# Optimization experiments

Measured on AMD Instinct MI355X. Metric: run time of the kernel, lower is better.

## Reference

```python
import jax, jax.numpy as jnp
import numpy as np

B, S, D = 1, 2048, 2048
H, HD = 32, 64  # num_heads, head_dim = hidden_size // num_heads


def setup_inputs() -> dict:
    key = jax.random.key(0)
    ks = jax.random.split(key, 7)
    sc = 0.02
    return {
        "hidden_states": jax.random.normal(ks[0], (B, S, D), dtype=jnp.float32),
        "Wq": jax.random.normal(ks[1], (D, D), dtype=jnp.float32) * sc,
        "Wk": jax.random.normal(ks[2], (D, D), dtype=jnp.float32) * sc,
        "Wv": jax.random.normal(ks[3], (D, D), dtype=jnp.float32) * sc,
        "Wf": jax.random.normal(ks[4], (H, D), dtype=jnp.float32) * sc,
        "bf": jax.random.normal(ks[5], (H,), dtype=jnp.float32),
        "Wo": jax.random.normal(ks[6], (D, D), dtype=jnp.float32) * sc,
    }


def reference(hidden_states, Wq, Wk, Wv, Wf, bf, Wo):
    x = hidden_states
    b, s, _ = x.shape
    # projections (nn.Linear: x @ W^T)
    q = (x @ Wq.T).reshape(b, s, H, HD)
    k = (x @ Wk.T).reshape(b, s, H, HD)
    v = (x @ Wv.T).reshape(b, s, H, HD)
    # per-head log forget gates, computed in float32 as in the torch module
    f = jax.nn.log_sigmoid((x @ Wf.T + bf).astype(jnp.float32))  # [b, s, H]
    # cumulative log decay; FoX bias D_ij = F_i - F_j (sum of log gates over (j, i])
    Fcum = jnp.cumsum(f, axis=1)               # [b, s, H]
    Fh = jnp.transpose(Fcum, (0, 2, 1))        # [b, H, s]
    scale = HD ** -0.5
    scores = jnp.einsum('bqhd,bkhd->bhqk', q, k).astype(jnp.float32) * scale
    scores = scores + Fh[:, :, :, None] - Fh[:, :, None, :]
    causal = jnp.tril(jnp.ones((s, s), dtype=bool))
    scores = jnp.where(causal[None, None], scores, -jnp.inf)
    p = jax.nn.softmax(scores, axis=-1).astype(q.dtype)  # [b, H, q, k]
    o = jnp.einsum('bhqk,bkhd->bqhd', p, v).reshape(b, s, D)
    return o @ Wo.T
```

## Files before the change

### kernel.cpp

```cpp
#include <hip/hip_runtime.h>
#include <stdint.h>

#define SEQ 2048
#define DM  2048
#define NH  32
#define HDIM 64

typedef unsigned short u16;
typedef short bf16x8 __attribute__((ext_vector_type(8)));
typedef float f32x4 __attribute__((ext_vector_type(4)));

__device__ __forceinline__ u16 f2bf(float f) {
    union { float f; uint32_t u; } v; v.f = f;
    uint32_t u = v.u;
    uint32_t r = (u + 0x7fffu + ((u >> 16) & 1u)) >> 16;
    return (u16)r;
}

#define GLOAD_LDS16(g, l) __builtin_amdgcn_global_load_lds( \
    (const __attribute__((address_space(1))) uint32_t*)(g), \
    (__attribute__((address_space(3))) uint32_t*)(l), 16, 0, 0)

__global__ __launch_bounds__(256) void cvt_bf16(
    const float* __restrict__ X, const float* __restrict__ Wq,
    const float* __restrict__ Wk, const float* __restrict__ Wv,
    const float* __restrict__ Wo,
    u16* __restrict__ Xb, u16* __restrict__ Wqb, u16* __restrict__ Wkb,
    u16* __restrict__ Wvb, u16* __restrict__ Wob)
{
    const int NV = (DM * SEQ) / 4;
    int idx = blockIdx.x * blockDim.x + threadIdx.x;
    int total = NV * 5;
    for (; idx < total; idx += gridDim.x * blockDim.x) {
        int arr = idx / NV, i = idx - arr * NV;
        const float4* s; u16* d;
        switch (arr) {
            case 0:  s = (const float4*)X;  d = Xb;  break;
            case 1:  s = (const float4*)Wq; d = Wqb; break;
            case 2:  s = (const float4*)Wk; d = Wkb; break;
            case 3:  s = (const float4*)Wv; d = Wvb; break;
            default: s = (const float4*)Wo; d = Wob; break;
        }
        float4 v = s[i];
        ushort4 o;
        o.x = f2bf(v.x); o.y = f2bf(v.y); o.z = f2bf(v.z); o.w = f2bf(v.w);
        *(ushort4*)(d + i * 4) = o;
    }
}

__global__ __launch_bounds__(256) void gates_gemm(
    const float* __restrict__ X, const float* __restrict__ Wf,
    float* __restrict__ Fpart)
{
    __shared__ float lX[64 * 68];
    __shared__ float lW[32 * 68];
    int s0 = blockIdx.x * 64;
    int kp = blockIdx.y;
    int tid = threadIdx.x;
    int h = tid & 31, sg = tid >> 5;
    float acc[8] = {0.f,0.f,0.f,0.f,0.f,0.f,0.f,0.f};
    for (int k0 = kp * 128; k0 < kp * 128 + 128; k0 += 64) {
        __syncthreads();
        {
            int r = tid >> 2, seg = tid & 3;
            const float4* src = (const float4*)(X + (size_t)(s0 + r) * DM + k0);
            float4* dst = (float4*)(&lX[r * 68]);
#pragma unroll
            for (int i = 0; i < 4; i++) dst[seg + 4 * i] = src[seg + 4 * i];
#pragma unroll
            for (int j = 0; j < 2; j++) {
                int ii = tid + j * 256;
                int wr_ = ii >> 4, wc_ = ii & 15;
                ((float4*)(&lW[wr_ * 68]))[wc_] =
                    ((const float4*)(Wf + (size_t)wr_ * DM + k0))[wc_];
            }
        }
        __syncthreads();
#pragma unroll
        for (int k4 = 0; k4 < 16; k4++) {
            float4 w = ((const float4*)(&lW[h * 68]))[k4];
#pragma unroll
            for (int i = 0; i < 8; i++) {
                float4 x = ((const float4*)(&lX[(sg + 8 * i) * 68]))[k4];
                acc[i] += x.x * w.x + x.y * w.y + x.z * w.z + x.w * w.w;
            }
        }
    }
#pragma unroll
    for (int i = 0; i < 8; i++)
        Fpart[(size_t)kp * NH * SEQ + h * SEQ + s0 + sg + 8 * i] = acc[i];
}

__global__ __launch_bounds__(256) void gates_scan(
    const float* __restrict__ Fpart, float* __restrict__ F,
    const float* __restrict__ bfp)
{
    __shared__ float lws[4];
    int h = blockIdx.x;
    int tid = threadIdx.x;
    int lane = tid & 63, wv = tid >> 6;
    float bb = bfp[h];
    float v[8] = {0.f,0.f,0.f,0.f,0.f,0.f,0.f,0.f};
#pragma unroll
    for (int kp = 0; kp < 16; kp++) {
        const float4* src = (const float4*)(Fpart + (size_t)kp * NH * SEQ + (size_t)h * SEQ);
        float4 a = src[tid * 2], b2 = src[tid * 2 + 1];
        v[0] += a.x;  v[1] += a.y;  v[2] += a.z;  v[3] += a.w;
        v[4] += b2.x; v[5] += b2.y; v[6] += b2.z; v[7] += b2.w;
    }
#pragma unroll
    for (int i = 0; i < 8; i++) {
        float g = v[i] + bb;
        v[i] = fminf(g, 0.f) - log1pf(expf(-fabsf(g)));
    }
#pragma unroll
    for (int i = 1; i < 8; i++) v[i] += v[i - 1];
    float tsum = v[7];
    float sc = tsum;
#pragma unroll
    for (int d = 1; d < 64; d <<= 1) {
        float t = __shfl_up(sc, d);
        if (lane >= d) sc += t;
    }
    if (lane == 63) lws[wv] = sc;
    __syncthreads();
    float woff = 0.f;
#pragma unroll
    for (int w2 = 0; w2 < 4; w2++) if (w2 < wv) woff += lws[w2];
    float off = woff + sc - tsum;
#pragma unroll
    for (int i = 0; i < 8; i++) v[i] += off;
    float4 o1 = {v[0], v[1], v[2], v[3]}, o2 = {v[4], v[5], v[6], v[7]};
    ((float4*)(F + (size_t)h * SEQ))[tid * 2] = o1;
    ((float4*)(F + (size_t)h * SEQ))[tid * 2 + 1] = o2;
}

__global__ __launch_bounds__(256, 3) void gemm_qkv(
    const u16* __restrict__ A,
    const u16* __restrict__ B0, const u16* __restrict__ B1, const u16* __restrict__ B2,
    u16* __restrict__ C0, u16* __restrict__ C1, u16* __restrict__ C2)
{
    __shared__ u16 lA[128 * 32];
    __shared__ u16 lB[128 * 32];
    const int K = DM, N = DM;
    int z = blockIdx.z;
    const u16* Bm = (z == 0) ? B0 : ((z == 1) ? B1 : B2);
    u16* Cm = (z == 0) ? C0 : ((z == 1) ? C1 : C2);
    int m0 = blockIdx.y * 128, n0 = blockIdx.x * 128;
    int tid = threadIdx.x;
    int wave = tid >> 6, lane = tid & 63, ln = lane & 15, quad = lane >> 4;
    int wr = (wave >> 1) * 64, wc = (wave & 1) * 64;

    f32x4 acc[4][4];
#pragma unroll
    for (int i = 0; i < 4; i++)
#pragma unroll
        for (int j = 0; j < 4; j++)
#pragma unroll
            for (int r = 0; r < 4; r++) acc[i][j][r] = 0.f;

    int srow = wave * 32 + (lane >> 2);
    int scol = (lane & 3) * 8;
    const u16* gA0 = &A[(size_t)(m0 + srow) * K + scol];
    const u16* gA1 = &A[(size_t)(m0 + srow + 16) * K + scol];
    const u16* gB0 = &Bm[(size_t)(n0 + srow) * K + scol];
    const u16* gB1 = &Bm[(size_t)(n0 + srow + 16) * K + scol];
    u16* dA0 = &lA[(wave * 32) * 32];
    u16* dA1 = &lA[(wave * 32 + 16) * 32];
    u16* dB0 = &lB[(wave * 32) * 32];
    u16* dB1 = &lB[(wave * 32 + 16) * 32];

    for (int kk0 = 0; kk0 < K / 32; kk0++) {
        __syncthreads();
        GLOAD_LDS16(gA0, dA0);
        GLOAD_LDS16(gA1, dA1);
        GLOAD_LDS16(gB0, dB0);
        GLOAD_LDS16(gB1, dB1);
        gA0 += 32; gA1 += 32; gB0 += 32; gB1 += 32;
        __syncthreads();
        bf16x8 af[4], bfr[4];
#pragma unroll
        for (int i = 0; i < 4; i++) af[i]  = *(const bf16x8*)(&lA[(wr + i * 16 + ln) * 32 + quad * 8]);
#pragma unroll
        for (int j = 0; j < 4; j++) bfr[j] = *(const bf16x8*)(&lB[(wc + j * 16 + ln) * 32 + quad * 8]);
#pragma unroll
        for (int i = 0; i < 4; i++)
#pragma unroll
            for (int j = 0; j < 4; j++)
                acc[i][j] = __builtin_amdgcn_mfma_f32_16x16x32_bf16(af[i], bfr[j], acc[i][j], 0, 0, 0);
    }

#pragma unroll
    for (int i = 0; i < 4; i++)
#pragma unroll
        for (int j = 0; j < 4; j++)
#pragma unroll
            for (int r = 0; r < 4; r++) {
                int row = m0 + wr + i * 16 + quad * 4 + r;
                int col = n0 + wc + j * 16 + ln;
                Cm[(size_t)row * N + col] = f2bf(acc[i][j][r]);
            }
}

__global__ __launch_bounds__(256, 3) void gemm_out(
    const u16* __restrict__ A, const u16* __restrict__ B,
    float* __restrict__ C)
{
    __shared__ u16 lA[128 * 32];
    __shared__ u16 lB[128 * 32];
    const int K = DM, N = DM;
    int m0 = blockIdx.y * 128, n0 = blockIdx.x * 128;
    int tid = threadIdx.x;
    int wave = tid >> 6, lane = tid & 63, ln = lane & 15, quad = lane >> 4;
    int wr = (wave >> 1) * 64, wc = (wave & 1) * 64;

    f32x4 acc[4][4];
#pragma unroll
    for (int i = 0; i < 4; i++)
#pragma unroll
        for (int j = 0; j < 4; j++)
#pragma unroll
            for (int r = 0; r < 4; r++) acc[i][j][r] = 0.f;

    int srow = wave * 32 + (lane >> 2);
    int scol = (lane & 3) * 8;
    const u16* gA0 = &A[(size_t)(m0 + srow) * K + scol];
    const u16* gA1 = &A[(size_t)(m0 + srow + 16) * K + scol];
    const u16* gB0 = &B[(size_t)(n0 + srow) * K + scol];
    const u16* gB1 = &B[(size_t)(n0 + srow + 16) * K + scol];
    u16* dA0 = &lA[(wave * 32) * 32];
    u16* dA1 = &lA[(wave * 32 + 16) * 32];
    u16* dB0 = &lB[(wave * 32) * 32];
    u16* dB1 = &lB[(wave * 32 + 16) * 32];

    for (int kk0 = 0; kk0 < K / 32; kk0++) {
        __syncthreads();
        GLOAD_LDS16(gA0, dA0);
        GLOAD_LDS16(gA1, dA1);
        GLOAD_LDS16(gB0, dB0);
        GLOAD_LDS16(gB1, dB1);
        gA0 += 32; gA1 += 32; gB0 += 32; gB1 += 32;
        __syncthreads();
        bf16x8 af[4], bfr[4];
#pragma unroll
        for (int i = 0; i < 4; i++) af[i]  = *(const bf16x8*)(&lA[(wr + i * 16 + ln) * 32 + quad * 8]);
#pragma unroll
        for (int j = 0; j < 4; j++) bfr[j] = *(const bf16x8*)(&lB[(wc + j * 16 + ln) * 32 + quad * 8]);
#pragma unroll
        for (int i = 0; i < 4; i++)
#pragma unroll
            for (int j = 0; j < 4; j++)
                acc[i][j] = __builtin_amdgcn_mfma_f32_16x16x32_bf16(af[i], bfr[j], acc[i][j], 0, 0, 0);
    }

#pragma unroll
    for (int i = 0; i < 4; i++)
#pragma unroll
        for (int j = 0; j < 4; j++)
#pragma unroll
            for (int r = 0; r < 4; r++) {
                int row = m0 + wr + i * 16 + quad * 4 + r;
                int col = n0 + wc + j * 16 + ln;
                C[(size_t)row * N + col] = acc[i][j][r];
            }
}

__global__ __launch_bounds__(256, 2) void attn_fox(
    const u16* __restrict__ Q, const u16* __restrict__ K,
    const u16* __restrict__ V, const float* __restrict__ F,
    u16* __restrict__ O)
{
    __shared__ u16 lK[64 * 72];
    __shared__ u16 lV[64 * 72];
    __shared__ u16 lP[4 * 16 * 72];
    __shared__ float lFq[64];
    __shared__ float lFk[64];

    int h = blockIdx.y;
    int q0 = blockIdx.x * 64;
    int tid = threadIdx.x;
    int wave = tid >> 6, lane = tid & 63, ln = lane & 15, quad = lane >> 4;
    const float scale = 0.125f;

    bf16x8 aq[2];
    int qrow = q0 + wave * 16 + ln;
#pragma unroll
    for (int kk = 0; kk < 2; kk++)
        aq[kk] = *(const bf16x8*)(&Q[(size_t)qrow * DM + h * HDIM + kk * 32 + quad * 8]);

    if (tid < 64) lFq[tid] = F[h * SEQ + q0 + tid];

    float m_run[4], l_run[4];
    f32x4 o_acc[4];
#pragma unroll
    for (int r = 0; r < 4; r++) { m_run[r] = -1e30f; l_run[r] = 0.f; }
#pragma unroll
    for (int jo = 0; jo < 4; jo++)
#pragma unroll
        for (int r = 0; r < 4; r++) o_acc[jo][r] = 0.f;

    float Fq0 = F[h * SEQ + q0];
    int nt = q0 / 64 + 1;
    u16* lPw = &lP[wave * 16 * 72];

    for (int kt = 0; kt < nt; kt++) {
        int kb = kt * 64;
        if (kt < nt - 1) {
            float Fkend = F[h * SEQ + kb + 63];
            if (Fq0 - Fkend < -50.f) continue;
        }
        __syncthreads();
        {
            int row = tid >> 3, seg = tid & 7;
            *(uint4*)(&lK[row * 72 + seg * 8])        = *(const uint4*)(&K[(size_t)(kb + row) * DM + h * HDIM + seg * 8]);
            *(uint4*)(&lK[(row + 32) * 72 + seg * 8]) = *(const uint4*)(&K[(size_t)(kb + row + 32) * DM + h * HDIM + seg * 8]);
        }
#pragma unroll
        for (int half = 0; half < 2; half++) {
            int job = half * 256 + tid;
            int kv = job & 63, hs = job >> 6;
            union { uint4 v; u16 e[8]; } tmp;
            tmp.v = *(const uint4*)(&V[(size_t)(kb + kv) * DM + h * HDIM + hs * 8]);
#pragma unroll
            for (int u = 0; u < 8; u++) lV[(hs * 8 + u) * 72 + kv] = tmp.e[u];
        }
        if (tid < 64) lFk[tid] = F[h * SEQ + kb + tid];
        __syncthreads();

        f32x4 s_acc[4];
#pragma unroll
        for (int j = 0; j < 4; j++)
#pragma unroll
            for (int r = 0; r < 4; r++) s_acc[j][r] = 0.f;
#pragma unroll
        for (int kk = 0; kk < 2; kk++)
#pragma unroll
            for (int j = 0; j < 4; j++) {
                bf16x8 bk = *(const bf16x8*)(&lK[(j * 16 + ln) * 72 + kk * 32 + quad * 8]);
                s_acc[j] = __builtin_amdgcn_mfma_f32_16x16x32_bf16(aq[kk], bk, s_acc[j], 0, 0, 0);
            }

        bool diag = (kt == nt - 1);
        int qbase = q0 + wave * 16 + quad * 4;
        float vv[4][4];
        float m_new[4];
#pragma unroll
        for (int r = 0; r < 4; r++) m_new[r] = -1e30f;
#pragma unroll
        for (int j = 0; j < 4; j++) {
            float fk = lFk[j * 16 + ln];
            int kglob = kb + j * 16 + ln;
#pragma unroll
            for (int r = 0; r < 4; r++) {
                float fq = lFq[wave * 16 + quad * 4 + r];
                float v = s_acc[j][r] * scale + (fq - fk);
                if (diag && kglob > qbase + r) v = -1e30f;
                vv[j][r] = v;
                m_new[r] = fmaxf(m_new[r], v);
            }
        }
#pragma unroll
        for (int r = 0; r < 4; r++) {
#pragma unroll
            for (int m = 1; m < 16; m <<= 1) m_new[r] = fmaxf(m_new[r], __shfl_xor(m_new[r], m));
        }
        float alpha[4];
#pragma unroll
        for (int r = 0; r < 4; r++) {
            float mt = fmaxf(m_run[r], m_new[r]);
            alpha[r] = expf(m_run[r] - mt);
            m_run[r] = mt;
        }
        float lsum[4] = {0.f, 0.f, 0.f, 0.f};
#pragma unroll
        for (int j = 0; j < 4; j++)
#pragma unroll
            for (int r = 0; r < 4; r++) {
                float pv = expf(vv[j][r] - m_run[r]);
                vv[j][r] = pv;
                lsum[r] += pv;
            }
#pragma unroll
        for (int r = 0; r < 4; r++) {
#pragma unroll
            for (int m = 1; m < 16; m <<= 1) lsum[r] += __shfl_xor(lsum[r], m);
            l_run[r] = l_run[r] * alpha[r] + lsum[r];
        }
#pragma unroll
        for (int jo = 0; jo < 4; jo++)
#pragma unroll
            for (int r = 0; r < 4; r++) o_acc[jo][r] *= alpha[r];

#pragma unroll
        for (int j = 0; j < 4; j++)
#pragma unroll
            for (int r = 0; r < 4; r++)
                lPw[(quad * 4 + r) * 72 + j * 16 + ln] = f2bf(vv[j][r]);
        __syncthreads();
        bf16x8 ap[2];
#pragma unroll
        for (int kk = 0; kk < 2; kk++)
            ap[kk] = *(const bf16x8*)(&lPw[ln * 72 + kk * 32 + quad * 8]);
#pragma unroll
        for (int kk = 0; kk < 2; kk++)
#pragma unroll
            for (int jo = 0; jo < 4; jo++) {
                bf16x8 bv = *(const bf16x8*)(&lV[(jo * 16 + ln) * 72 + kk * 32 + quad * 8]);
                o_acc[jo] = __builtin_amdgcn_mfma_f32_16x16x32_bf16(ap[kk], bv, o_acc[jo], 0, 0, 0);
            }
    }

#pragma unroll
    for (int r = 0; r < 4; r++) {
        float inv = 1.f / l_run[r];
        int row = q0 + wave * 16 + quad * 4 + r;
#pragma unroll
        for (int jo = 0; jo < 4; jo++)
            O[(size_t)row * DM + h * HDIM + jo * 16 + ln] = f2bf(o_acc[jo][r] * inv);
    }
}

extern "C" void kernel_launch(void* const* d_in, const int* in_sizes, int n_in,
                              void* d_out, int out_size, void* d_ws, size_t ws_size,
                              hipStream_t stream)
{
    const float* X   = (const float*)d_in[0];
    const float* Wq  = (const float*)d_in[1];
    const float* Wk  = (const float*)d_in[2];
    const float* Wv  = (const float*)d_in[3];
    const float* Wf  = (const float*)d_in[4];
    const float* bfp = (const float*)d_in[5];
    const float* Wo  = (const float*)d_in[6];
    float* out = (float*)d_out;

    char* ws = (char*)d_ws;
    const size_t MB8 = (size_t)DM * SEQ * 2;
    u16* Xb  = (u16*)(ws + 0 * MB8);
    u16* Wqb = (u16*)(ws + 1 * MB8);
    u16* Wkb = (u16*)(ws + 2 * MB8);
    u16* Wvb = (u16*)(ws + 3 * MB8);
    u16* Wob = (u16*)(ws + 4 * MB8);
    u16* Qb  = (u16*)(ws + 5 * MB8);
    u16* Kb  = (u16*)(ws + 6 * MB8);
    u16* Vb  = (u16*)(ws + 7 * MB8);
    u16* Ob  = (u16*)(ws + 8 * MB8);
    float* Fb = (float*)(ws + 9 * MB8);
    float* Fpart = (float*)(ws + 8 * MB8);

    cvt_bf16<<<dim3(4096), dim3(256), 0, stream>>>(X, Wq, Wk, Wv, Wo, Xb, Wqb, Wkb, Wvb, Wob);
    gates_gemm<<<dim3(32, 16), dim3(256), 0, stream>>>(X, Wf, Fpart);
    gates_scan<<<dim3(NH), dim3(256), 0, stream>>>(Fpart, Fb, bfp);
    gemm_qkv<<<dim3(16, 16, 3), dim3(256), 0, stream>>>(Xb, Wqb, Wkb, Wvb, Qb, Kb, Vb);
    attn_fox<<<dim3(SEQ / 64, NH), dim3(256), 0, stream>>>(Qb, Kb, Vb, Fb, Ob);
    gemm_out<<<dim3(16, 16), dim3(256), 0, stream>>>(Ob, Wob, out);
}
```

Measured before the change: 273.4 us.

## Write V transposed from QKV GEMM and read K/V directly from global in attention

The QKV GEMM now stores V transposed (head-dim major, sequence contiguous), so the attention kernel can load MFMA B-fragments for K and V straight from global memory. This drops the per-tile LDS staging of K and V, the scalar transpose scatter into LDS, and two block-wide barriers per key tile, and raises occupancy to 3 blocks. F values are also read directly into registers. The conversion kernel's grid is split by array index to avoid per-element division. The cost is that each wave now issues its own uncoalesced strided global reads of K and V fragments, and these reads are repeated across the four waves instead of shared through LDS.

```diff
diff --git a/kernel.cpp b/kernel.cpp
--- a/kernel.cpp
+++ b/kernel.cpp
@@ -29,18 +29,16 @@
     u16* __restrict__ Wvb, u16* __restrict__ Wob)
 {
     const int NV = (DM * SEQ) / 4;
-    int idx = blockIdx.x * blockDim.x + threadIdx.x;
-    int total = NV * 5;
-    for (; idx < total; idx += gridDim.x * blockDim.x) {
-        int arr = idx / NV, i = idx - arr * NV;
-        const float4* s; u16* d;
-        switch (arr) {
-            case 0:  s = (const float4*)X;  d = Xb;  break;
-            case 1:  s = (const float4*)Wq; d = Wqb; break;
-            case 2:  s = (const float4*)Wk; d = Wkb; break;
-            case 3:  s = (const float4*)Wv; d = Wvb; break;
-            default: s = (const float4*)Wo; d = Wob; break;
-        }
+    int arr = blockIdx.y;
+    const float4* s; u16* d;
+    switch (arr) {
+        case 0:  s = (const float4*)X;  d = Xb;  break;
+        case 1:  s = (const float4*)Wq; d = Wqb; break;
+        case 2:  s = (const float4*)Wk; d = Wkb; break;
+        case 3:  s = (const float4*)Wv; d = Wvb; break;
+        default: s = (const float4*)Wo; d = Wob; break;
+    }
+    for (int i = blockIdx.x * blockDim.x + threadIdx.x; i < NV; i += gridDim.x * blockDim.x) {
         float4 v = s[i];
         ushort4 o;
         o.x = f2bf(v.x); o.y = f2bf(v.y); o.z = f2bf(v.z); o.w = f2bf(v.w);
@@ -190,16 +188,30 @@
                 acc[i][j] = __builtin_amdgcn_mfma_f32_16x16x32_bf16(af[i], bfr[j], acc[i][j], 0, 0, 0);
     }
 
-#pragma unroll
-    for (int i = 0; i < 4; i++)
-#pragma unroll
-        for (int j = 0; j < 4; j++)
-#pragma unroll
-            for (int r = 0; r < 4; r++) {
-                int row = m0 + wr + i * 16 + quad * 4 + r;
+    if (z == 2) {
+#pragma unroll
+        for (int i = 0; i < 4; i++)
+#pragma unroll
+            for (int j = 0; j < 4; j++) {
                 int col = n0 + wc + j * 16 + ln;
-                Cm[(size_t)row * N + col] = f2bf(acc[i][j][r]);
-            }
+                int row0 = m0 + wr + i * 16 + quad * 4;
+                ushort4 pk;
+                pk.x = f2bf(acc[i][j][0]); pk.y = f2bf(acc[i][j][1]);
+                pk.z = f2bf(acc[i][j][2]); pk.w = f2bf(acc[i][j][3]);
+                *(ushort4*)(&Cm[(size_t)col * SEQ + row0]) = pk;
+            }
+    } else {
+#pragma unroll
+        for (int i = 0; i < 4; i++)
+#pragma unroll
+            for (int j = 0; j < 4; j++)
+#pragma unroll
+                for (int r = 0; r < 4; r++) {
+                    int row = m0 + wr + i * 16 + quad * 4 + r;
+                    int col = n0 + wc + j * 16 + ln;
+                    Cm[(size_t)row * N + col] = f2bf(acc[i][j][r]);
+                }
+    }
 }
 
 __global__ __launch_bounds__(256, 3) void gemm_out(
@@ -265,22 +277,19 @@
             }
 }
 
-__global__ __launch_bounds__(256, 2) void attn_fox(
+__global__ __launch_bounds__(256, 3) void attn_fox(
     const u16* __restrict__ Q, const u16* __restrict__ K,
-    const u16* __restrict__ V, const float* __restrict__ F,
+    const u16* __restrict__ Vt, const float* __restrict__ F,
     u16* __restrict__ O)
 {
-    __shared__ u16 lK[64 * 72];
-    __shared__ u16 lV[64 * 72];
     __shared__ u16 lP[4 * 16 * 72];
-    __shared__ float lFq[64];
-    __shared__ float lFk[64];
 
     int h = blockIdx.y;
     int q0 = blockIdx.x * 64;
     int tid = threadIdx.x;
     int wave = tid >> 6, lane = tid & 63, ln = lane & 15, quad = lane >> 4;
     const float scale = 0.125f;
+    const float* Fh = F + (size_t)h * SEQ;
 
     bf16x8 aq[2];
     int qrow = q0 + wave * 16 + ln;
@@ -288,7 +297,9 @@
     for (int kk = 0; kk < 2; kk++)
         aq[kk] = *(const bf16x8*)(&Q[(size_t)qrow * DM + h * HDIM + kk * 32 + quad * 8]);
 
-    if (tid < 64) lFq[tid] = F[h * SEQ + q0 + tid];
+    float fq[4];
+#pragma unroll
+    for (int r = 0; r < 4; r++) fq[r] = Fh[q0 + wave * 16 + quad * 4 + r];
 
     float m_run[4], l_run[4];
     f32x4 o_acc[4];
@@ -299,33 +310,15 @@
 #pragma unroll
         for (int r = 0; r < 4; r++) o_acc[jo][r] = 0.f;
 
-    float Fq0 = F[h * SEQ + q0];
+    float Fq0 = Fh[q0];
     int nt = q0 / 64 + 1;
     u16* lPw = &lP[wave * 16 * 72];
 
     for (int kt = 0; kt < nt; kt++) {
         int kb = kt * 64;
         if (kt < nt - 1) {
-            float Fkend = F[h * SEQ + kb + 63];
-            if (Fq0 - Fkend < -50.f) continue;
-        }
-        __syncthreads();
-        {
-            int row = tid >> 3, seg = tid & 7;
-            *(uint4*)(&lK[row * 72 + seg * 8])        = *(const uint4*)(&K[(size_t)(kb + row) * DM + h * HDIM + seg * 8]);
-            *(uint4*)(&lK[(row + 32) * 72 + seg * 8]) = *(const uint4*)(&K[(size_t)(kb + row + 32) * DM + h * HDIM + seg * 8]);
-        }
-#pragma unroll
-        for (int half = 0; half < 2; half++) {
-            int job = half * 256 + tid;
-            int kv = job & 63, hs = job >> 6;
-            union { uint4 v; u16 e[8]; } tmp;
-            tmp.v = *(const uint4*)(&V[(size_t)(kb + kv) * DM + h * HDIM + hs * 8]);
-#pragma unroll
-            for (int u = 0; u < 8; u++) lV[(hs * 8 + u) * 72 + kv] = tmp.e[u];
-        }
-        if (tid < 64) lFk[tid] = F[h * SEQ + kb + tid];
-        __syncthreads();
+            if (Fq0 - Fh[kb + 63] < -50.f) continue;
+        }
 
         f32x4 s_acc[4];
 #pragma unroll
@@ -336,7 +329,7 @@
         for (int kk = 0; kk < 2; kk++)
 #pragma unroll
             for (int j = 0; j < 4; j++) {
-                bf16x8 bk = *(const bf16x8*)(&lK[(j * 16 + ln) * 72 + kk * 32 + quad * 8]);
+                bf16x8 bk = *(const bf16x8*)(&K[(size_t)(kb + j * 16 + ln) * DM + h * HDIM + kk * 32 + quad * 8]);
                 s_acc[j] = __builtin_amdgcn_mfma_f32_16x16x32_bf16(aq[kk], bk, s_acc[j], 0, 0, 0);
             }
 
@@ -348,12 +341,11 @@
         for (int r = 0; r < 4; r++) m_new[r] = -1e30f;
 #pragma unroll
         for (int j = 0; j < 4; j++) {
-            float fk = lFk[j * 16 + ln];
+            float fk = Fh[kb + j * 16 + ln];
             int kglob = kb + j * 16 + ln;
 #pragma unroll
             for (int r = 0; r < 4; r++) {
-                float fq = lFq[wave * 16 + quad * 4 + r];
-                float v = s_acc[j][r] * scale + (fq - fk);
+                float v = s_acc[j][r] * scale + (fq[r] - fk);
                 if (diag && kglob > qbase + r) v = -1e30f;
                 vv[j][r] = v;
                 m_new[r] = fmaxf(m_new[r], v);
@@ -401,11 +393,12 @@
 #pragma unroll
         for (int kk = 0; kk < 2; kk++)
             ap[kk] = *(const bf16x8*)(&lPw[ln * 72 + kk * 32 + quad * 8]);
+
 #pragma unroll
         for (int kk = 0; kk < 2; kk++)
 #pragma unroll
             for (int jo = 0; jo < 4; jo++) {
-                bf16x8 bv = *(const bf16x8*)(&lV[(jo * 16 + ln) * 72 + kk * 32 + quad * 8]);
+                bf16x8 bv = *(const bf16x8*)(&Vt[(size_t)(h * HDIM + jo * 16 + ln) * SEQ + kb + kk * 32 + quad * 8]);
                 o_acc[jo] = __builtin_amdgcn_mfma_f32_16x16x32_bf16(ap[kk], bv, o_acc[jo], 0, 0, 0);
             }
     }
@@ -442,15 +435,15 @@
     u16* Wob = (u16*)(ws + 4 * MB8);
     u16* Qb  = (u16*)(ws + 5 * MB8);
     u16* Kb  = (u16*)(ws + 6 * MB8);
-    u16* Vb  = (u16*)(ws + 7 * MB8);
+    u16* Vtb = (u16*)(ws + 7 * MB8);
     u16* Ob  = (u16*)(ws + 8 * MB8);
     float* Fb = (float*)(ws + 9 * MB8);
     float* Fpart = (float*)(ws + 8 * MB8);
 
-    cvt_bf16<<<dim3(4096), dim3(256), 0, stream>>>(X, Wq, Wk, Wv, Wo, Xb, Wqb, Wkb, Wvb, Wob);
+    cvt_bf16<<<dim3(1024, 5), dim3(256), 0, stream>>>(X, Wq, Wk, Wv, Wo, Xb, Wqb, Wkb, Wvb, Wob);
     gates_gemm<<<dim3(32, 16), dim3(256), 0, stream>>>(X, Wf, Fpart);
     gates_scan<<<dim3(NH), dim3(256), 0, stream>>>(Fpart, Fb, bfp);
-    gemm_qkv<<<dim3(16, 16, 3), dim3(256), 0, stream>>>(Xb, Wqb, Wkb, Wvb, Qb, Kb, Vb);
-    attn_fox<<<dim3(SEQ / 64, NH), dim3(256), 0, stream>>>(Qb, Kb, Vb, Fb, Ob);
+    gemm_qkv<<<dim3(16, 16, 3), dim3(256), 0, stream>>>(Xb, Wqb, Wkb, Wvb, Qb, Kb, Vtb);
+    attn_fox<<<dim3(SEQ / 64, NH), dim3(256), 0, stream>>>(Qb, Kb, Vtb, Fb, Ob);
     gemm_out<<<dim3(16, 16), dim3(256), 0, stream>>>(Ob, Wob, out);
 }
```

After: 281.6 us. +3.0%, slower.
